# Kernel tuning notes

Measured on AMD Instinct MI355X. Metric: run time of the kernel, lower is better.

Reference implementation:

```python
import jax, jax.numpy as jnp
import numpy as np

EMBED_DIM = 768
NUM_HEADS = 12
HEAD_DIM = EMBED_DIM // NUM_HEADS
MAX_REL = 50
B, L = 4, 1024


def setup_inputs() -> dict:
    key = jax.random.key(0)
    ks = jax.random.split(key, 8)
    query = jax.random.normal(ks[0], (B, L, EMBED_DIM), dtype=jnp.float32)
    k_in = jax.random.normal(ks[1], (B, L, EMBED_DIM), dtype=jnp.float32)
    v_in = jax.random.normal(ks[2], (B, L, EMBED_DIM), dtype=jnp.float32)
    # monotone float timestamps per batch (arange fill)
    patch_indices = jnp.arange(B * L, dtype=jnp.float32).reshape(B, L)
    std = 1.0 / np.sqrt(EMBED_DIM)
    in_proj_w = jax.random.normal(ks[3], (3 * EMBED_DIM, EMBED_DIM), dtype=jnp.float32) * std
    in_proj_b = jnp.zeros((3 * EMBED_DIM,), dtype=jnp.float32)
    out_proj_w = jax.random.normal(ks[4], (EMBED_DIM, EMBED_DIM), dtype=jnp.float32) * std
    out_proj_b = jnp.zeros((EMBED_DIM,), dtype=jnp.float32)
    rel_bias = jax.random.truncated_normal(ks[5], -2.0, 2.0, (NUM_HEADS, 2 * MAX_REL + 1), dtype=jnp.float32) * 0.1
    return {"query": query, "key": k_in, "value": v_in, "patch_indices": patch_indices,
            "in_proj_w": in_proj_w, "in_proj_b": in_proj_b,
            "out_proj_w": out_proj_w, "out_proj_b": out_proj_b, "rel_bias": rel_bias}


def _attention(query, patch_indices, in_proj_w, in_proj_b, out_proj_w, out_proj_b, rel_bias):
    Bq, Lq, D = query.shape
    H, hd, M = NUM_HEADS, HEAD_DIM, MAX_REL
    qkv = query @ in_proj_w.T + in_proj_b            # [B,L,3D]
    q, k, v = jnp.split(qkv, 3, axis=-1)
    q = q.reshape(Bq, Lq, H, hd).transpose(0, 2, 1, 3) * (hd ** -0.5)
    k = k.reshape(Bq, Lq, H, hd).transpose(0, 2, 1, 3)
    v = v.reshape(Bq, Lq, H, hd).transpose(0, 2, 1, 3)
    scores = jnp.einsum('bhld,bhmd->bhlm', q, k)     # [B,H,L,L]
    # sequence-position relative bias
    idxs = jnp.arange(Lq)
    rel_pos = jnp.clip(idxs[None, :] - idxs[:, None], -M, M) + M   # [L,L]
    scores = scores + rel_bias[:, rel_pos][None]                   # [1,H,L,L]
    # data-dependent relative-time bias
    deltas = patch_indices[:, 1:] - patch_indices[:, :-1]          # [B,L-1]
    dt = jnp.nanmedian(deltas, axis=1)
    dt = jnp.where(jnp.isfinite(dt) & (dt > 0), dt, 1.0)[:, None, None]
    rel_time = patch_indices[:, :, None] - patch_indices[:, None, :]  # [B,L,L]
    invalid = jnp.isnan(rel_time) | (rel_time < -M) | (rel_time > M)
    rel_time = jnp.where(invalid, 0.0, rel_time)
    rel_idx = (jnp.clip(jnp.round(rel_time / dt), -M, M) + M).astype(jnp.int32)  # [B,L,L]
    bias = jnp.take(rel_bias, rel_idx, axis=1)       # [H,B,L,L]
    scores = scores + jnp.moveaxis(bias, 0, 1)       # [B,H,L,L]
    probs = jax.nn.softmax(scores, axis=-1)
    out = jnp.einsum('bhlm,bhmd->bhld', probs, v)
    out = out.transpose(0, 2, 1, 3).reshape(Bq, Lq, D)
    return out @ out_proj_w.T + out_proj_b


def reference(query, key, value, patch_indices, in_proj_w, in_proj_b, out_proj_w, out_proj_b, rel_bias):
    # NOTE: the original module ignores key/value and builds qkv from query.
    return _attention(query, patch_indices, in_proj_w, in_proj_b, out_proj_w, out_proj_b, rel_bias)
```

## Files before the change

### kernel.cpp

```cpp
#include <hip/hip_runtime.h>
#include <hip/hip_bf16.h>

#define BB 4
#define LL 1024
#define DD 768
#define HH 12
#define HD 64
#define MREL 50
#define NBIAS 101
#define GK 768
#define STR 72
#define BXS 68

#define NEG_INF (-__builtin_inff())

#define QB_F   ((size_t)0)
#define KB_F   ((size_t)1572864)
#define VTB_F  ((size_t)3145728)
#define XBF_F  ((size_t)4718592)
#define WIBF_F ((size_t)6291456)
#define WOBF_F ((size_t)7176192)
#define BIDX_F ((size_t)7471104)
#define DT_F   ((size_t)9568256)

#define NQ4  (BB*LL*DD)
#define NWI4 (3*DD*DD)

typedef __attribute__((ext_vector_type(8)))  short bf16x8;
typedef __attribute__((ext_vector_type(4)))  float f32x4;
typedef __attribute__((ext_vector_type(16))) float f32x16;

__device__ __forceinline__ unsigned short f2bf(float f) {
    unsigned u = __float_as_uint(f);
    u += 0x7fffu + ((u >> 16) & 1u);
    return (unsigned short)(u >> 16);
}

__device__ __forceinline__ void gload_lds16(const void* g, void* l) {
    __builtin_amdgcn_global_load_lds(
        (const __attribute__((address_space(1))) void*)g,
        (__attribute__((address_space(3))) void*)l, 16, 0, 0);
}

__global__ __launch_bounds__(256) void cvt3_kernel(
    const float* __restrict__ q, const float* __restrict__ wi, const float* __restrict__ wo,
    unsigned short* __restrict__ qd_, unsigned short* __restrict__ wid,
    unsigned short* __restrict__ wod) {
    int i = (blockIdx.x * 256 + threadIdx.x) * 4;
    const float* src; unsigned short* dst; int off;
    if (i < NQ4)              { src = q;  dst = qd_; off = i; }
    else if (i < NQ4 + NWI4)  { src = wi; dst = wid; off = i - NQ4; }
    else                      { src = wo; dst = wod; off = i - NQ4 - NWI4; }
    float4 v = *(const float4*)&src[off];
    ushort4 o;
    o.x = f2bf(v.x); o.y = f2bf(v.y); o.z = f2bf(v.z); o.w = f2bf(v.w);
    *(ushort4*)&dst[off] = o;
}

__global__ __launch_bounds__(256) void dt_kernel(const float* __restrict__ patch,
                                                 float* __restrict__ dt) {
    __shared__ __align__(16) float del[1024];
    __shared__ __align__(16) unsigned long long key64[1024];
    __shared__ int nvalid;
    __shared__ float acc;
    int b = blockIdx.x, tid = threadIdx.x;
    if (tid == 0) { nvalid = 0; acc = 0.f; }
    __syncthreads();
    int cnt = 0;
#pragma unroll
    for (int r = 0; r < 4; ++r) {
        int i = tid + r * 256;
        float v = __builtin_nanf("");
        if (i < LL - 1) {
            v = patch[b * LL + i + 1] - patch[b * LL + i];
            if (v == v) ++cnt;
        }
        del[i] = v;
        unsigned bits = (v == v) ? __float_as_uint(v) : 0x7FC00000u;
        unsigned ordk = (bits & 0x80000000u) ? ~bits : (bits | 0x80000000u);
        key64[i] = ((unsigned long long)ordk << 10) | (unsigned)i;
    }
    atomicAdd(&nvalid, cnt);
    __syncthreads();
    int i0 = tid, i1 = tid + 256, i2 = tid + 512, i3 = tid + 768;
    float v0 = del[i0], v1 = del[i1], v2 = del[i2], v3 = del[i3];
    unsigned long long k0 = key64[i0], k1 = key64[i1], k2 = key64[i2], k3 = key64[i3];
    int c0 = 0, c1 = 0, c2 = 0, c3 = 0;
#define CMPK(kx) { unsigned long long _k = (kx); \
    c0 += (_k < k0) ? 1 : 0; c1 += (_k < k1) ? 1 : 0; \
    c2 += (_k < k2) ? 1 : 0; c3 += (_k < k3) ? 1 : 0; }
    for (int j = 0; j < 1024; j += 8) {
        ulonglong2 a = *(const ulonglong2*)&key64[j];
        ulonglong2 bq = *(const ulonglong2*)&key64[j + 2];
        ulonglong2 cq = *(const ulonglong2*)&key64[j + 4];
        ulonglong2 dq = *(const ulonglong2*)&key64[j + 6];
        CMPK(a.x); CMPK(a.y); CMPK(bq.x); CMPK(bq.y);
        CMPK(cq.x); CMPK(cq.y); CMPK(dq.x); CMPK(dq.y);
    }
#undef CMPK
    int n = nvalid;
#define FIN(vr, cr) if (vr == vr) { \
    if (n & 1) { if (cr == n / 2) atomicAdd(&acc, vr); } \
    else { if (cr == n / 2 - 1 || cr == n / 2) atomicAdd(&acc, 0.5f * vr); } }
    FIN(v0, c0); FIN(v1, c1); FIN(v2, c2); FIN(v3, c3);
#undef FIN
    __syncthreads();
    if (tid == 0) {
        float m = acc;
        float res = (n > 0 && m == m && fabsf(m) != __builtin_inff() && m > 0.f) ? m : 1.0f;
        dt[b] = res;
    }
}

__global__ __launch_bounds__(256) void bidx_kernel(const float* __restrict__ patch,
                                                   const float* __restrict__ dtb,
                                                   unsigned short* __restrict__ bidx) {
    int flat = (blockIdx.x * 256 + threadIdx.x) * 8;
    int b = flat >> 20;
    int rem = flat & 1048575;
    int i = rem >> 10;
    int j0 = rem & 1023;
    float pi = patch[b * LL + i];
    float inv_dt = 1.0f / dtb[b];
    float4 pa = *(const float4*)&patch[b * LL + j0];
    float4 pb4 = *(const float4*)&patch[b * LL + j0 + 4];
    unsigned out[4];
#define MK(pj, jofs, dst, shift) { \
    int d = (j0 + jofs) - i; d = d < -MREL ? -MREL : (d > MREL ? MREL : d); \
    float rt = pi - (pj); \
    if (!(rt == rt) || rt < -(float)MREL || rt > (float)MREL) rt = 0.f; \
    float fr = fminf(fmaxf(rintf(rt * inv_dt), -(float)MREL), (float)MREL); \
    unsigned u = (unsigned)(d + MREL) | (((unsigned)((int)fr + MREL)) << 8); \
    dst |= (u << shift); }
    unsigned t;
    t = 0; MK(pa.x, 0, t, 0); MK(pa.y, 1, t, 16); out[0] = t;
    t = 0; MK(pa.z, 2, t, 0); MK(pa.w, 3, t, 16); out[1] = t;
    t = 0; MK(pb4.x, 4, t, 0); MK(pb4.y, 5, t, 16); out[2] = t;
    t = 0; MK(pb4.z, 6, t, 0); MK(pb4.w, 7, t, 16); out[3] = t;
#undef MK
    *(uint4*)&bidx[flat] = *(uint4*)&out[0];
}

#define GEMM_PROLOG()                                                          \
    __shared__ unsigned short As[2 * 128 * 64];                                \
    __shared__ unsigned short Bs[2 * 128 * 64];                                \
    int tid = threadIdx.x;                                                     \
    int m0 = blockIdx.x << 7, n0 = blockIdx.y << 7;                            \
    int lane = tid & 63, w = tid >> 6;                                         \
    int wm = (w >> 1) << 6, wn = (w & 1) << 6;                                 \
    int srow = tid >> 3;                                                       \
    int scol = (tid & 7) << 3;                                                 \
    const unsigned short* Ag = Ab + (size_t)(m0 + srow) * GK + scol;           \
    const unsigned short* Bg = Wb + (size_t)(n0 + srow) * GK + scol;           \
    f32x4 acc[4][4];                                                           \
    _Pragma("unroll") for (int i = 0; i < 4; ++i)                              \
        _Pragma("unroll") for (int j = 0; j < 4; ++j)                          \
            acc[i][j] = (f32x4){0.f, 0.f, 0.f, 0.f};                           \
    int qd_ = lane >> 4;                                                       \
    int rA = wm + (lane & 15), rB = wn + (lane & 15);                          \
    _Pragma("unroll") for (int r = 0; r < 4; ++r) {                            \
        gload_lds16(Ag + (size_t)(r * 32) * GK, As + tid * 8 + r * 2048);      \
        gload_lds16(Bg + (size_t)(r * 32) * GK, Bs + tid * 8 + r * 2048);      \
    }                                                                          \
    int cur = 0;                                                               \
    for (int kc = 0; kc < GK; kc += 64) {                                      \
        __syncthreads();                                                       \
        if (kc + 64 < GK) {                                                    \
            int nxt = cur ^ 1;                                                 \
            _Pragma("unroll") for (int r = 0; r < 4; ++r) {                    \
                gload_lds16(Ag + (size_t)(r * 32) * GK + kc + 64,              \
                            As + nxt * 8192 + tid * 8 + r * 2048);             \
                gload_lds16(Bg + (size_t)(r * 32) * GK + kc + 64,              \
                            Bs + nxt * 8192 + tid * 8 + r * 2048);             \
            }                                                                  \
        }                                                                      \
        const unsigned short* Ac = As + cur * 8192;                            \
        const unsigned short* Bc = Bs + cur * 8192;                            \
        _Pragma("unroll") for (int ks = 0; ks < 2; ++ks) {                     \
            bf16x8 af[4], bfr[4];                                              \
            _Pragma("unroll") for (int t = 0; t < 4; ++t)                      \
                af[t] = *(const bf16x8*)&Ac[(rA + t * 16) * 64 + ks * 32 + qd_ * 8]; \
            _Pragma("unroll") for (int t = 0; t < 4; ++t)                      \
                bfr[t] = *(const bf16x8*)&Bc[(rB + t * 16) * 64 + ks * 32 + qd_ * 8]; \
            _Pragma("unroll") for (int i = 0; i < 4; ++i)                      \
                _Pragma("unroll") for (int j = 0; j < 4; ++j)                  \
                    acc[i][j] = __builtin_amdgcn_mfma_f32_16x16x32_bf16(       \
                        af[i], bfr[j], acc[i][j], 0, 0, 0);                    \
        }                                                                      \
        cur ^= 1;                                                              \
    }                                                                          \
    int colL = lane & 15, rq = lane >> 4;

__global__ __launch_bounds__(256) void qkv_gemm(
    const unsigned short* __restrict__ Ab, const unsigned short* __restrict__ Wb,
    const float* __restrict__ bias,
    unsigned short* __restrict__ qb, unsigned short* __restrict__ kb,
    unsigned short* __restrict__ vtb) {
    GEMM_PROLOG();
    int sec = n0 / DD;
    float scale = (sec == 0) ? 0.125f : 1.0f;
#pragma unroll
    for (int j = 0; j < 4; ++j) {
        int n = n0 + wn + j * 16 + colL;
        int d768 = n - sec * DD;
        int hh = d768 >> 6, dd = d768 & 63;
        float bn = bias[n];
#pragma unroll
        for (int i = 0; i < 4; ++i) {
            int rowb = m0 + wm + i * 16 + rq * 4;
#pragma unroll
            for (int r = 0; r < 4; ++r) {
                int m = rowb + r;
                int bidx = m >> 10, l = m & 1023;
                unsigned short val = f2bf((acc[i][j][r] + bn) * scale);
                if (sec == 0)
                    qb[(((size_t)bidx * HH + hh) * LL + l) * HD + dd] = val;
                else if (sec == 1)
                    kb[(((size_t)bidx * HH + hh) * LL + l) * HD + dd] = val;
                else
                    vtb[(((size_t)bidx * HH + hh) * HD + dd) * LL + l] = val;
            }
        }
    }
}

__global__ __launch_bounds__(256) void out_gemm(
    const unsigned short* __restrict__ Ab, const unsigned short* __restrict__ Wb,
    const float* __restrict__ bias, float* __restrict__ C) {
    GEMM_PROLOG();
#pragma unroll
    for (int j = 0; j < 4; ++j) {
        int n = n0 + wn + j * 16 + colL;
        float bn = bias[n];
#pragma unroll
        for (int i = 0; i < 4; ++i) {
            int rowb = m0 + wm + i * 16 + rq * 4;
#pragma unroll
            for (int r = 0; r < 4; ++r)
                C[(size_t)(rowb + r) * DD + n] = acc[i][j][r] + bn;
        }
    }
}

__global__ __launch_bounds__(256) void attn_kernel(
    const unsigned short* __restrict__ QB, const unsigned short* __restrict__ KB,
    const unsigned short* __restrict__ VTB, const unsigned short* __restrict__ BIDX,
    const float* __restrict__ relb, unsigned short* __restrict__ aout) {
    __shared__ unsigned short Ks[64 * STR];
    __shared__ unsigned short Vt[64 * STR];
    __shared__ unsigned short Ps[64 * STR];
    __shared__ unsigned short Bxs[64 * BXS];
    __shared__ float sb[NBIAS];
    __shared__ float pmax_s[128];
    __shared__ float psum_s[128];
    __shared__ float alpha_s[64];
    __shared__ float linv_s[64];
    int tid = threadIdx.x;
    int w = tid >> 6, lane = tid & 63, li = lane & 31, qd = lane >> 5;
    int jt = w & 1, it = w >> 1;
    int bh = blockIdx.x, b = bh / HH, h = bh - b * HH;
    int q0 = blockIdx.y << 6;
    if (tid < NBIAS) sb[tid] = relb[h * NBIAS + tid];
    int i_loc = it * 32 + li;
    int i_abs = q0 + i_loc;
    bf16x8 kq[4];
    const unsigned short* qrow = QB + ((size_t)bh * LL + i_abs) * HD + qd * 8;
#pragma unroll
    for (int ks = 0; ks < 4; ++ks) kq[ks] = *(const bf16x8*)(qrow + ks * 16);
    float m_old = NEG_INF, l_run = 0.f;
    f32x16 O;
#pragma unroll
    for (int r = 0; r < 16; ++r) O[r] = 0.f;
    int srow = tid >> 3, sc = (tid & 7) << 3;
    const unsigned short* kgb = KB + (size_t)bh * LL * HD;
    const unsigned short* vgb = VTB + (size_t)bh * HD * LL;
    const unsigned short* bxg = BIDX + ((size_t)b << 20) + (size_t)q0 * 1024;
    for (int kt = 0; kt < 16; ++kt) {
        __syncthreads();
#pragma unroll
        for (int rep = 0; rep < 2; ++rep) {
            int r = srow + rep * 32;
            bf16x8 kv = *(const bf16x8*)(kgb + (size_t)(kt * 64 + r) * HD + sc);
            *(bf16x8*)&Ks[r * STR + sc] = kv;
            bf16x8 vv = *(const bf16x8*)(vgb + (size_t)r * LL + kt * 64 + sc);
            *(bf16x8*)&Vt[r * STR + sc] = vv;
            bf16x8 bx = *(const bf16x8*)(bxg + (size_t)r * 1024 + kt * 64 + sc);
            *(bf16x8*)&Bxs[r * BXS + sc] = bx;
        }
        __syncthreads();
        f32x16 st;
#pragma unroll
        for (int r = 0; r < 16; ++r) st[r] = 0.f;
#pragma unroll
        for (int ks = 0; ks < 4; ++ks) {
            bf16x8 ak = *(const bf16x8*)&Ks[(jt * 32 + li) * STR + ks * 16 + qd * 8];
            st = __builtin_amdgcn_mfma_f32_32x32x16_bf16(ak, kq[ks], st, 0, 0, 0);
        }
        float pm = NEG_INF;
#pragma unroll
        for (int g = 0; g < 4; ++g) {
            ushort4 bi = *(const ushort4*)&Bxs[i_loc * BXS + jt * 32 + g * 8 + qd * 4];
#pragma unroll
            for (int q = 0; q < 4; ++q) {
                int r = g * 4 + q;
                unsigned u = (q == 0) ? bi.x : (q == 1) ? bi.y : (q == 2) ? bi.z : bi.w;
                float v = st[r] + sb[u & 0xffu] + sb[u >> 8];
                st[r] = v;
                pm = fmaxf(pm, v);
            }
        }
        pm = fmaxf(pm, __shfl_xor(pm, 32));
        if (qd == 0) pmax_s[jt * 64 + i_loc] = pm;
        __syncthreads();
        float mt = fmaxf(pmax_s[i_loc], pmax_s[64 + i_loc]);
        float mnew = fmaxf(m_old, mt);
        float alpha = __expf(m_old - mnew);
        m_old = mnew;
        float rs = 0.f;
        unsigned pu[8];
#pragma unroll
        for (int pr = 0; pr < 8; ++pr) {
            float p0 = __expf(st[2 * pr] - mnew);
            float p1 = __expf(st[2 * pr + 1] - mnew);
            unsigned u0 = __float_as_uint(p0);
            u0 += 0x7fffu + ((u0 >> 16) & 1u); u0 &= 0xffff0000u;
            unsigned u1 = __float_as_uint(p1);
            u1 += 0x7fffu + ((u1 >> 16) & 1u); u1 &= 0xffff0000u;
            rs += __uint_as_float(u0);
            rs += __uint_as_float(u1);
            pu[pr] = (u0 >> 16) | u1;
        }
        rs += __shfl_xor(rs, 32);
        if (qd == 0) {
            psum_s[jt * 64 + i_loc] = rs;
            if (jt == 0) alpha_s[i_loc] = alpha;
        }
#pragma unroll
        for (int pr = 0; pr < 8; ++pr) {
            int r = pr * 2;
            int jl = (r & 3) + ((r >> 2) << 3) + (qd << 2);
            *(unsigned*)&Ps[i_loc * STR + jt * 32 + jl] = pu[pr];
        }
        __syncthreads();
        if (jt == 0) l_run = l_run * alpha + psum_s[i_loc] + psum_s[64 + i_loc];
#pragma unroll
        for (int r = 0; r < 16; ++r) {
            int row = (r & 3) + ((r >> 2) << 3) + (qd << 2);
            O[r] *= alpha_s[it * 32 + row];
        }
#pragma unroll
        for (int ks = 0; ks < 4; ++ks) {
            bf16x8 ap = *(const bf16x8*)&Ps[i_loc * STR + ks * 16 + qd * 8];
            bf16x8 bv = *(const bf16x8*)&Vt[(jt * 32 + li) * STR + ks * 16 + qd * 8];
            O = __builtin_amdgcn_mfma_f32_32x32x16_bf16(ap, bv, O, 0, 0, 0);
        }
    }
    if (jt == 0 && qd == 0) linv_s[i_loc] = 1.0f / l_run;
    __syncthreads();
#pragma unroll
    for (int r = 0; r < 16; ++r) {
        int row = (r & 3) + ((r >> 2) << 3) + (qd << 2);
        float v = O[r] * linv_s[it * 32 + row];
        aout[(size_t)(b * LL + q0 + it * 32 + row) * DD + h * HD + jt * 32 + li] = f2bf(v);
    }
}

extern "C" void kernel_launch(void* const* d_in, const int* in_sizes, int n_in,
                              void* d_out, int out_size, void* d_ws, size_t ws_size,
                              hipStream_t stream) {
    const float* query    = (const float*)d_in[0];
    const float* patch    = (const float*)d_in[3];
    const float* in_w     = (const float*)d_in[4];
    const float* in_b     = (const float*)d_in[5];
    const float* out_w    = (const float*)d_in[6];
    const float* out_b    = (const float*)d_in[7];
    const float* rel_bias = (const float*)d_in[8];
    float* ws  = (float*)d_ws;
    float* out = (float*)d_out;

    unsigned short* qb   = (unsigned short*)(ws + QB_F);
    unsigned short* kb   = (unsigned short*)(ws + KB_F);
    unsigned short* vtb  = (unsigned short*)(ws + VTB_F);
    unsigned short* xbf  = (unsigned short*)(ws + XBF_F);
    unsigned short* wibf = (unsigned short*)(ws + WIBF_F);
    unsigned short* wobf = (unsigned short*)(ws + WOBF_F);
    unsigned short* bidx = (unsigned short*)(ws + BIDX_F);

    dt_kernel<<<BB, 256, 0, stream>>>(patch, ws + DT_F);
    bidx_kernel<<<2048, 256, 0, stream>>>(patch, ws + DT_F, bidx);
    cvt3_kernel<<<5376, 256, 0, stream>>>(query, in_w, out_w, xbf, wibf, wobf);
    qkv_gemm<<<dim3(32, 18), 256, 0, stream>>>(xbf, wibf, in_b, qb, kb, vtb);
    attn_kernel<<<dim3(BB * HH, LL / 64), 256, 0, stream>>>(
        qb, kb, vtb, bidx, rel_bias, xbf);
    out_gemm<<<dim3(32, 6), 256, 0, stream>>>(xbf, wobf, out_b, out);
}
```

Measured before the change: 234.5 us.

## Shrink GEMM tiles for more blocks and drop LDS double buffering

Replaces the 128x128 double-buffered GEMM tile with smaller tiles: 64x128 for the QKV projection and 64x64 for the output projection. This doubles and quadruples the grid sizes respectively, so more of the GPU's CUs are occupied. The LDS double-buffer prefetch is removed in favour of a single buffer with two barriers per k-step, which gives up overlap between global loads and MFMA work. The aim is better CU utilisation for these small GEMMs, at the cost of more redundant operand loads and exposed memory latency.

```diff
diff --git a/kernel.cpp b/kernel.cpp
--- a/kernel.cpp
+++ b/kernel.cpp
@@ -141,53 +141,40 @@
     *(uint4*)&bidx[flat] = *(uint4*)&out[0];
 }
 
-#define GEMM_PROLOG()                                                          \
-    __shared__ unsigned short As[2 * 128 * 64];                                \
-    __shared__ unsigned short Bs[2 * 128 * 64];                                \
+#define GEMM_CORE(TN_, RB_, NT_)                                               \
+    __shared__ unsigned short As[64 * 64];                                     \
+    __shared__ unsigned short Bs[TN_ * 64];                                    \
     int tid = threadIdx.x;                                                     \
-    int m0 = blockIdx.x << 7, n0 = blockIdx.y << 7;                            \
+    int m0 = blockIdx.x << 6, n0 = blockIdx.y * TN_;                           \
     int lane = tid & 63, w = tid >> 6;                                         \
-    int wm = (w >> 1) << 6, wn = (w & 1) << 6;                                 \
-    int srow = tid >> 3;                                                       \
-    int scol = (tid & 7) << 3;                                                 \
+    int wn = w * (TN_ / 4);                                                    \
+    int srow = tid >> 3, scol = (tid & 7) << 3;                                \
     const unsigned short* Ag = Ab + (size_t)(m0 + srow) * GK + scol;           \
     const unsigned short* Bg = Wb + (size_t)(n0 + srow) * GK + scol;           \
-    f32x4 acc[4][4];                                                           \
+    f32x4 acc[4][NT_];                                                         \
     _Pragma("unroll") for (int i = 0; i < 4; ++i)                              \
-        _Pragma("unroll") for (int j = 0; j < 4; ++j)                          \
+        _Pragma("unroll") for (int j = 0; j < NT_; ++j)                        \
             acc[i][j] = (f32x4){0.f, 0.f, 0.f, 0.f};                           \
     int qd_ = lane >> 4;                                                       \
-    int rA = wm + (lane & 15), rB = wn + (lane & 15);                          \
-    _Pragma("unroll") for (int r = 0; r < 4; ++r) {                            \
-        gload_lds16(Ag + (size_t)(r * 32) * GK, As + tid * 8 + r * 2048);      \
-        gload_lds16(Bg + (size_t)(r * 32) * GK, Bs + tid * 8 + r * 2048);      \
-    }                                                                          \
-    int cur = 0;                                                               \
+    int rA = lane & 15, rB = wn + (lane & 15);                                 \
     for (int kc = 0; kc < GK; kc += 64) {                                      \
         __syncthreads();                                                       \
-        if (kc + 64 < GK) {                                                    \
-            int nxt = cur ^ 1;                                                 \
-            _Pragma("unroll") for (int r = 0; r < 4; ++r) {                    \
-                gload_lds16(Ag + (size_t)(r * 32) * GK + kc + 64,              \
-                            As + nxt * 8192 + tid * 8 + r * 2048);             \
-                gload_lds16(Bg + (size_t)(r * 32) * GK + kc + 64,              \
-                            Bs + nxt * 8192 + tid * 8 + r * 2048);             \
-            }                                                                  \
-        }                                                                      \
-        const unsigned short* Ac = As + cur * 8192;                            \
-        const unsigned short* Bc = Bs + cur * 8192;                            \
+        _Pragma("unroll") for (int r = 0; r < 2; ++r)                          \
+            gload_lds16(Ag + (size_t)(r * 32) * GK + kc, As + tid * 8 + r * 2048); \
+        _Pragma("unroll") for (int r = 0; r < RB_; ++r)                        \
+            gload_lds16(Bg + (size_t)(r * 32) * GK + kc, Bs + tid * 8 + r * 2048); \
+        __syncthreads();                                                       \
         _Pragma("unroll") for (int ks = 0; ks < 2; ++ks) {                     \
-            bf16x8 af[4], bfr[4];                                              \
+            bf16x8 af[4], bfr[NT_];                                            \
             _Pragma("unroll") for (int t = 0; t < 4; ++t)                      \
-                af[t] = *(const bf16x8*)&Ac[(rA + t * 16) * 64 + ks * 32 + qd_ * 8]; \
-            _Pragma("unroll") for (int t = 0; t < 4; ++t)                      \
-                bfr[t] = *(const bf16x8*)&Bc[(rB + t * 16) * 64 + ks * 32 + qd_ * 8]; \
+                af[t] = *(const bf16x8*)&As[(rA + t * 16) * 64 + ks * 32 + qd_ * 8]; \
+            _Pragma("unroll") for (int t = 0; t < NT_; ++t)                    \
+                bfr[t] = *(const bf16x8*)&Bs[(rB + t * 16) * 64 + ks * 32 + qd_ * 8]; \
             _Pragma("unroll") for (int i = 0; i < 4; ++i)                      \
-                _Pragma("unroll") for (int j = 0; j < 4; ++j)                  \
+                _Pragma("unroll") for (int j = 0; j < NT_; ++j)                \
                     acc[i][j] = __builtin_amdgcn_mfma_f32_16x16x32_bf16(       \
                         af[i], bfr[j], acc[i][j], 0, 0, 0);                    \
         }                                                                      \
-        cur ^= 1;                                                              \
     }                                                                          \
     int colL = lane & 15, rq = lane >> 4;
 
@@ -196,18 +183,18 @@
     const float* __restrict__ bias,
     unsigned short* __restrict__ qb, unsigned short* __restrict__ kb,
     unsigned short* __restrict__ vtb) {
-    GEMM_PROLOG();
+    GEMM_CORE(128, 4, 2);
     int sec = n0 / DD;
     float scale = (sec == 0) ? 0.125f : 1.0f;
 #pragma unroll
-    for (int j = 0; j < 4; ++j) {
+    for (int j = 0; j < 2; ++j) {
         int n = n0 + wn + j * 16 + colL;
         int d768 = n - sec * DD;
         int hh = d768 >> 6, dd = d768 & 63;
         float bn = bias[n];
 #pragma unroll
         for (int i = 0; i < 4; ++i) {
-            int rowb = m0 + wm + i * 16 + rq * 4;
+            int rowb = m0 + i * 16 + rq * 4;
 #pragma unroll
             for (int r = 0; r < 4; ++r) {
                 int m = rowb + r;
@@ -227,17 +214,16 @@
 __global__ __launch_bounds__(256) void out_gemm(
     const unsigned short* __restrict__ Ab, const unsigned short* __restrict__ Wb,
     const float* __restrict__ bias, float* __restrict__ C) {
-    GEMM_PROLOG();
-#pragma unroll
-    for (int j = 0; j < 4; ++j) {
-        int n = n0 + wn + j * 16 + colL;
+    GEMM_CORE(64, 2, 1);
+    {
+        int n = n0 + wn + colL;
         float bn = bias[n];
 #pragma unroll
         for (int i = 0; i < 4; ++i) {
-            int rowb = m0 + wm + i * 16 + rq * 4;
+            int rowb = m0 + i * 16 + rq * 4;
 #pragma unroll
             for (int r = 0; r < 4; ++r)
-                C[(size_t)(rowb + r) * DD + n] = acc[i][j][r] + bn;
+                C[(size_t)(rowb + r) * DD + n] = acc[i][0][r] + bn;
         }
     }
 }
@@ -389,8 +375,8 @@
     dt_kernel<<<BB, 256, 0, stream>>>(patch, ws + DT_F);
     bidx_kernel<<<2048, 256, 0, stream>>>(patch, ws + DT_F, bidx);
     cvt3_kernel<<<5376, 256, 0, stream>>>(query, in_w, out_w, xbf, wibf, wobf);
-    qkv_gemm<<<dim3(32, 18), 256, 0, stream>>>(xbf, wibf, in_b, qb, kb, vtb);
+    qkv_gemm<<<dim3(64, 18), 256, 0, stream>>>(xbf, wibf, in_b, qb, kb, vtb);
     attn_kernel<<<dim3(BB * HH, LL / 64), 256, 0, stream>>>(
         qb, kb, vtb, bidx, rel_bias, xbf);
-    out_gemm<<<dim3(32, 6), 256, 0, stream>>>(xbf, wobf, out_b, out);
-}
+    out_gemm<<<dim3(64, 12), 256, 0, stream>>>(xbf, wobf, out_b, out);
+}
```

Result: faster. 224.8 us (-4.1%).
